# Performance work log

Measured on AMD Instinct MI355X. Metric: run time of the kernel, lower is better.

The kernel has to match this reference:

```python
import jax, jax.numpy as jnp
import numpy as np

B, S, D, H = 4, 2048, 1024, 16
HD = D // H


def setup_inputs() -> dict:
    key = jax.random.key(0)
    k1, k2, k3 = jax.random.split(key, 3)
    x = jax.random.normal(k1, (B, S, D), dtype=jnp.float32)
    w_qkv = jax.random.normal(k2, (D, 3 * D), dtype=jnp.float32) * (1.0 / np.sqrt(D))
    w_out = jax.random.normal(k3, (D, D), dtype=jnp.float32) * (1.0 / np.sqrt(D))
    return {"x": x, "w_qkv": w_qkv, "w_out": w_out}


def reference(x, w_qkv, w_out):
    bsz, seq_len, d = x.shape
    qkv = x @ w_qkv  # [B, S, 3D]
    q, k, v = jnp.split(qkv, 3, axis=-1)
    # [B, H, S, HD]
    q = q.reshape(bsz, seq_len, H, HD).transpose(0, 2, 1, 3)
    k = k.reshape(bsz, seq_len, H, HD).transpose(0, 2, 1, 3)
    v = v.reshape(bsz, seq_len, H, HD).transpose(0, 2, 1, 3)
    scale = 1.0 / np.sqrt(HD)
    scores = jnp.einsum('bhqd,bhkd->bhqk', q, k) * scale  # [B, H, S, S]
    causal = jnp.tril(jnp.ones((seq_len, seq_len), dtype=bool))
    scores = jnp.where(causal[None, None], scores, -jnp.inf)
    weights = jax.nn.softmax(scores, axis=-1)
    ctx = jnp.einsum('bhqk,bhkd->bhqd', weights, v)
    ctx = ctx.transpose(0, 2, 1, 3).reshape(bsz, seq_len, d)
    return ctx @ w_out
```

## Files before the change

### kernel.cpp

```cpp
#include <hip/hip_runtime.h>
#include <stdint.h>

typedef unsigned short u16;
typedef __attribute__((ext_vector_type(4))) float f32x4;
typedef __attribute__((ext_vector_type(8))) __bf16 bf16x8;
typedef __attribute__((ext_vector_type(8))) u16 u16x8;
typedef __attribute__((ext_vector_type(4))) u16 u16x4;

static constexpr int kB = 4, kS = 2048, kD = 1024, kH = 16, kHD = 64;
static constexpr int M1 = kB * kS;
static constexpr int N1 = 3 * kD;
static constexpr int K1 = kD;

#define SCLF 0.18033688011112042f
#define MFMA16(a, b, c) __builtin_amdgcn_mfma_f32_16x16x32_bf16((a), (b), (c), 0, 0, 0)

union U4 { unsigned u[4]; bf16x8 v; };

__device__ __forceinline__ u16 f2bf(float f) {
  union { float f; uint32_t u; } c; c.f = f;
  uint32_t u = c.u + 0x7FFFu + ((c.u >> 16) & 1u);
  return (u16)(u >> 16);
}

__device__ __forceinline__ unsigned pkbf(float a, float b) {
  union { __bf16 h[2]; unsigned u; } c;
  c.h[0] = (__bf16)a; c.h[1] = (__bf16)b;
  return c.u;
}

__device__ __forceinline__ void gload_lds16(const u16* g, u16* l) {
  __builtin_amdgcn_global_load_lds(
      (const __attribute__((address_space(1))) unsigned int*)g,
      (__attribute__((address_space(3))) unsigned int*)l, 16, 0, 0);
}

__global__ __launch_bounds__(256) void k_cast_x(const float* __restrict__ x,
                                                u16* __restrict__ o) {
  int i = (blockIdx.x * 256 + threadIdx.x) * 4;
  f32x4 v = *(const f32x4*)(x + i);
  u16x4 r;
  r[0] = f2bf(v[0]); r[1] = f2bf(v[1]); r[2] = f2bf(v[2]); r[3] = f2bf(v[3]);
  *(u16x4*)(o + i) = r;
}

__global__ __launch_bounds__(256) void k_transpose_cast(const float* __restrict__ w,
                                                        u16* __restrict__ wt,
                                                        int K, int N) {
  __shared__ float t[32][33];
  const int n0 = blockIdx.x * 32, k0 = blockIdx.y * 32;
  const int tx = threadIdx.x & 31, ty = threadIdx.x >> 5;
  for (int r = ty; r < 32; r += 8)
    t[r][tx] = w[(size_t)(k0 + r) * N + n0 + tx];
  __syncthreads();
  for (int r = ty; r < 32; r += 8)
    wt[(size_t)(n0 + r) * K + k0 + tx] = f2bf(t[tx][r]);
}

template <int MODE>
__global__ __launch_bounds__(256) void k_gemm_bt(const u16* __restrict__ A,
                                                 const u16* __restrict__ BT,
                                                 u16* __restrict__ obf,
                                                 float* __restrict__ of,
                                                 int M, int N, int K) {
  typedef __attribute__((ext_vector_type(4))) float f4;
  __shared__ __align__(16) u16 As[128 * 32];
  __shared__ __align__(16) u16 Bs[128 * 32];
  const int tid = threadIdx.x;
  const int wave = tid >> 6, lane = tid & 63;
  const int l15 = lane & 15, l16 = lane >> 4;

  const int bid = blockIdx.y * gridDim.x + blockIdx.x;
  const int qch = (gridDim.x * gridDim.y) >> 3;
  const int swz = (bid & 7) * qch + (bid >> 3);
  const int row0 = (swz / gridDim.x) * 128, col0 = (swz % gridDim.x) * 128;
  const int wm = (wave >> 1) * 64, wn = (wave & 1) * 64;

  f4 acc[4][4];
#pragma unroll
  for (int i = 0; i < 4; ++i)
#pragma unroll
    for (int j = 0; j < 4; ++j) acc[i][j] = f4{0.f, 0.f, 0.f, 0.f};

  const int e0 = wave * 512 + lane * 8;
  const int r0 = e0 >> 5, c0 = e0 & 31;
  const int e1 = e0 + 2048;
  const int r1 = e1 >> 5, c1 = e1 & 31;
  const u16* Ab = A + (size_t)row0 * K;
  const u16* Bb = BT + (size_t)col0 * K;

  for (int kt = 0; kt < K; kt += 32) {
    gload_lds16(Ab + (size_t)r0 * K + kt + c0, &As[wave * 512]);
    gload_lds16(Ab + (size_t)r1 * K + kt + c1, &As[2048 + wave * 512]);
    gload_lds16(Bb + (size_t)r0 * K + kt + c0, &Bs[wave * 512]);
    gload_lds16(Bb + (size_t)r1 * K + kt + c1, &Bs[2048 + wave * 512]);
    __syncthreads();
    bf16x8 af[4], bfv[4];
#pragma unroll
    for (int f = 0; f < 4; ++f) {
      af[f]  = *(const bf16x8*)&As[(wm + f * 16 + l15) * 32 + l16 * 8];
      bfv[f] = *(const bf16x8*)&Bs[(wn + f * 16 + l15) * 32 + l16 * 8];
    }
#pragma unroll
    for (int fm = 0; fm < 4; ++fm)
#pragma unroll
      for (int fn = 0; fn < 4; ++fn)
        acc[fm][fn] = MFMA16(af[fm], bfv[fn], acc[fm][fn]);
    __syncthreads();
  }

#pragma unroll
  for (int fm = 0; fm < 4; ++fm)
#pragma unroll
    for (int fn = 0; fn < 4; ++fn) {
      const int n = col0 + wn + fn * 16 + l15;
#pragma unroll
      for (int j = 0; j < 4; ++j) {
        const int m = row0 + wm + fm * 16 + l16 * 4 + j;
        float v = acc[fm][fn][j];
        if constexpr (MODE == 0) {
          const int which = n >> 10, d = n & 1023;
          const int h = d >> 6, hd = d & 63;
          const int b = m >> 11, s = m & 2047;
          if (which == 0) v *= SCLF;
          obf[((((size_t)which * 4 + b) * 16 + h) * 2048 + s) * 64 + hd] = f2bf(v);
        } else {
          of[(size_t)m * N + n] = v;
        }
      }
    }
}

__global__ __launch_bounds__(512, 4) void k_attn(const u16* __restrict__ Qg,
                                                 const u16* __restrict__ Kg,
                                                 const u16* __restrict__ Vg,
                                                 u16* __restrict__ ctx) {
  __shared__ __align__(16) u16 Ks[2][64 * 64];
  __shared__ __align__(16) unsigned Vt[2][2048];

  const int bid = blockIdx.x;
  const int xcd = bid & 7, i2 = bid >> 3;
  const int bh = xcd * 8 + (i2 & 7);
  const int p = i2 >> 3;
  const int bb = bh >> 4, hh = bh & 15;
  const int tid = threadIdx.x;
  const int wave = tid >> 6, lane = tid & 63;
  const int l15 = lane & 15, l16 = lane >> 4;

  const u16* Qb = Qg + (size_t)bh * kS * kHD;
  const u16* Kb = Kg + (size_t)bh * kS * kHD;
  const u16* Vb = Vg + (size_t)bh * kS * kHD;

  const int kkey = tid >> 3, ksl = tid & 7;
  const int do4 = tid & 15, kp = tid >> 4;
  const int srcA = ((l16 & 1) << 5) + l15;
  const int srcB = srcA + 16;
  const bool lo16 = (l16 < 2);

  unsigned voff[4];
#pragma unroll
  for (int i = 0; i < 4; ++i) {
    const int d = do4 * 4 + i;
    voff[i] = d * 32 + (kp ^ ((((d & 7) ^ (d >> 3))) << 2));
  }
  const u16* ksrc = Kb + (size_t)kkey * 64 + (ksl ^ (kkey & 7)) * 8;

  for (int phase = 0; phase < 2; ++phase) {
    const int qsup = phase ? (15 - p) : p;
    const int qstart = qsup * 128 + wave * 16;
    const int ntiles = 2 * qsup + 2;

    bf16x8 bq[2];
#pragma unroll
    for (int ds = 0; ds < 2; ++ds)
      bq[ds] = *(const bf16x8*)(Qb + (size_t)(qstart + l15) * 64 + ds * 32 + l16 * 8);

    f32x4 acc[4];
#pragma unroll
    for (int i = 0; i < 4; ++i) acc[i] = f32x4{0.f, 0.f, 0.f, 0.f};
    float mrow = -3e38f, lrowh = 0.f;

    __syncthreads();

    u16x4 va, vb;
    {
      const u16* vs = Vb + (size_t)(2 * kp) * 64 + do4 * 4;
      va = *(const u16x4*)vs; vb = *(const u16x4*)(vs + 64);
    }
#pragma unroll
    for (int i = 0; i < 4; ++i)
      Vt[0][voff[i]] = (unsigned)va[i] | ((unsigned)vb[i] << 16);
    {
      const u16* vs = Vb + (size_t)(64 + 2 * kp) * 64 + do4 * 4;
      va = *(const u16x4*)vs; vb = *(const u16x4*)(vs + 64);
    }
    gload_lds16(ksrc, &Ks[0][wave * 512]);

    for (int t = 0; t < ntiles; ++t) {
      const int kv0 = t * 64;
      __syncthreads();

      if (t + 1 < ntiles) {
        const int nb = (t + 1) & 1;
#pragma unroll
        for (int i = 0; i < 4; ++i)
          Vt[nb][voff[i]] = (unsigned)va[i] | ((unsigned)vb[i] << 16);
        gload_lds16(ksrc + (size_t)(t + 1) * 64 * 64, &Ks[nb][wave * 512]);
        if (t + 2 < ntiles) {
          const u16* vs = Vb + (size_t)((t + 2) * 64 + 2 * kp) * 64 + do4 * 4;
          va = *(const u16x4*)vs; vb = *(const u16x4*)(vs + 64);
        }
      }

      if (kv0 > qstart + 15) continue;

      const u16* Ksb = &Ks[t & 1][0];
      const unsigned* Vtb = &Vt[t & 1][0];
      const int qv = qstart + l15;

#pragma unroll
      for (int c = 0; c < 2; ++c) {
        const int kb = kv0 + 32 * c;
        if (kb > qstart + 15) continue;

        f32x4 st0 = f32x4{0.f, 0.f, 0.f, 0.f}, st1 = st0;
        __builtin_amdgcn_s_setprio(1);
#pragma unroll
        for (int ds = 0; ds < 2; ++ds) {
          const int slot = ((ds * 4 + l16) ^ (l15 & 7)) * 8;
          bf16x8 ak0 = *(const bf16x8*)&Ksb[(c * 32 + l15) * 64 + slot];
          st0 = MFMA16(ak0, bq[ds], st0);
          bf16x8 ak1 = *(const bf16x8*)&Ksb[(c * 32 + 16 + l15) * 64 + slot];
          st1 = MFMA16(ak1, bq[ds], st1);
        }
        __builtin_amdgcn_s_setprio(0);

        float tl;
        if (kb + 31 > qstart) {
#pragma unroll
          for (int j = 0; j < 4; ++j) {
            const int key = kb + l16 * 4 + j;
            st0[j] = (key <= qv) ? st0[j] : -3e38f;
            st1[j] = (key + 16 <= qv) ? st1[j] : -3e38f;
          }
        }
        tl = fmaxf(fmaxf(fmaxf(st0[0], st0[1]), fmaxf(st0[2], st0[3])),
                   fmaxf(fmaxf(st1[0], st1[1]), fmaxf(st1[2], st1[3])));

        float mn;
        if (__all(tl <= mrow + 8.0f)) {
          mn = mrow;
        } else {
          float tj = fmaxf(tl, __shfl_xor(tl, 16, 64));
          tj = fmaxf(tj, __shfl_xor(tj, 32, 64));
          mn = fmaxf(mrow, tj);
          const float al = exp2f(mrow - mn);
          mrow = mn;
          lrowh *= al;
#pragma unroll
          for (int i = 0; i < 4; ++i)
#pragma unroll
            for (int j = 0; j < 4; ++j) acc[i][j] *= al;
        }

#pragma unroll
        for (int j = 0; j < 4; ++j) {
          st0[j] = exp2f(st0[j] - mn);
          st1[j] = exp2f(st1[j] - mn);
        }
        lrowh += ((st0[0] + st0[1]) + (st0[2] + st0[3])) +
                 ((st1[0] + st1[1]) + (st1[2] + st1[3]));

        const unsigned a0  = pkbf(st0[0], st0[1]), a0b = pkbf(st0[2], st0[3]);
        const unsigned a1  = pkbf(st1[0], st1[1]), a1b = pkbf(st1[2], st1[3]);
        const unsigned sA0  = __shfl(a0, srcA, 64),  sA0b = __shfl(a0b, srcA, 64);
        const unsigned sB0  = __shfl(a0, srcB, 64),  sB0b = __shfl(a0b, srcB, 64);
        const unsigned sA1  = __shfl(a1, srcA, 64),  sA1b = __shfl(a1b, srcA, 64);
        const unsigned sB1  = __shfl(a1, srcB, 64),  sB1b = __shfl(a1b, srcB, 64);
        U4 f;
        f.u[0] = lo16 ? sA0 : sA1;  f.u[1] = lo16 ? sA0b : sA1b;
        f.u[2] = lo16 ? sB0 : sB1;  f.u[3] = lo16 ? sB0b : sB1b;

        __builtin_amdgcn_s_setprio(1);
#pragma unroll
        for (int dg = 0; dg < 4; ++dg) {
          const int d = dg * 16 + l15;
          const int addr = d * 32 + ((c * 16 + l16 * 4) ^ ((((d & 7) ^ (d >> 3))) << 2));
          const bf16x8 vf = *(const bf16x8*)&Vtb[addr];
          acc[dg] = MFMA16(vf, f.v, acc[dg]);
        }
        __builtin_amdgcn_s_setprio(0);
      }
    }

    float l2 = lrowh + __shfl_xor(lrowh, 16, 64);
    const float lrow = l2 + __shfl_xor(l2, 32, 64);
    const float rl = 1.0f / lrow;
    u16* orow = ctx + ((size_t)bb * kS + (qstart + l15)) * kD + hh * 64;
#pragma unroll
    for (int dg = 0; dg < 4; ++dg) {
      u16x4 pk;
#pragma unroll
      for (int j = 0; j < 4; ++j) pk[j] = f2bf(acc[dg][j] * rl);
      *(u16x4*)&orow[dg * 16 + l16 * 4] = pk;
    }
  }
}

extern "C" void kernel_launch(void* const* d_in, const int* in_sizes, int n_in,
                              void* d_out, int out_size, void* d_ws, size_t ws_size,
                              hipStream_t stream) {
  const float* x     = (const float*)d_in[0];
  const float* w_qkv = (const float*)d_in[1];
  const float* w_out = (const float*)d_in[2];
  float* out = (float*)d_out;

  u16* ws    = (u16*)d_ws;
  u16* x_bf  = ws;
  u16* wqkvT = x_bf + (size_t)M1 * K1;
  u16* woutT = wqkvT + (size_t)N1 * K1;
  u16* qkv   = woutT + (size_t)kD * kD;
  u16* ctx   = qkv + (size_t)3 * kB * kH * kS * kHD;

  k_cast_x<<<M1 * K1 / 1024, 256, 0, stream>>>(x, x_bf);
  k_transpose_cast<<<dim3(N1 / 32, K1 / 32), 256, 0, stream>>>(w_qkv, wqkvT, K1, N1);
  k_transpose_cast<<<dim3(kD / 32, kD / 32), 256, 0, stream>>>(w_out, woutT, kD, kD);

  k_gemm_bt<0><<<dim3(N1 / 128, M1 / 128), 256, 0, stream>>>(x_bf, wqkvT, qkv, nullptr,
                                                             M1, N1, K1);

  const u16* Qg = qkv;
  const u16* Kg = qkv + (size_t)kB * kH * kS * kHD;
  const u16* Vg = qkv + (size_t)2 * kB * kH * kS * kHD;
  k_attn<<<dim3(512), 512, 0, stream>>>(Qg, Kg, Vg, ctx);

  k_gemm_bt<1><<<dim3(kD / 128, M1 / 128), 256, 0, stream>>>(ctx, woutT, nullptr, out,
                                                             M1, kD, K1);
}
```

Baseline: 206.1 us.

## Rewrite GEMM with 128x256 tiles, triple-buffered async LDS loads and swizzle

Restructures the projection GEMMs to use 512-thread blocks with 128x256 output tiles, a K-step of 64, and a three-stage LDS ring. Loads go straight to LDS and are overlapped with MFMA compute using explicit vmcnt waits and a single barrier per step. An XOR swizzle on LDS columns avoids bank conflicts, and MFMA priority is raised. The aim is to hide global memory latency and raise arithmetic intensity per block, at the cost of higher LDS use (144KB per block) and fewer blocks in flight.

```diff
diff --git a/kernel.cpp b/kernel.cpp
--- a/kernel.cpp
+++ b/kernel.cpp
@@ -58,55 +58,91 @@
 }
 
 template <int MODE>
-__global__ __launch_bounds__(256) void k_gemm_bt(const u16* __restrict__ A,
+__global__ __launch_bounds__(512) void k_gemm_bt(const u16* __restrict__ A,
                                                  const u16* __restrict__ BT,
                                                  u16* __restrict__ obf,
                                                  float* __restrict__ of,
                                                  int M, int N, int K) {
-  typedef __attribute__((ext_vector_type(4))) float f4;
-  __shared__ __align__(16) u16 As[128 * 32];
-  __shared__ __align__(16) u16 Bs[128 * 32];
+  __shared__ __align__(16) u16 Asb[3][128 * 64];
+  __shared__ __align__(16) u16 Bsb[3][256 * 64];
+
   const int tid = threadIdx.x;
   const int wave = tid >> 6, lane = tid & 63;
   const int l15 = lane & 15, l16 = lane >> 4;
 
-  const int bid = blockIdx.y * gridDim.x + blockIdx.x;
-  const int qch = (gridDim.x * gridDim.y) >> 3;
+  const int bid = blockIdx.x;
+  const int qch = gridDim.x >> 3;
   const int swz = (bid & 7) * qch + (bid >> 3);
-  const int row0 = (swz / gridDim.x) * 128, col0 = (swz % gridDim.x) * 128;
-  const int wm = (wave >> 1) * 64, wn = (wave & 1) * 64;
-
-  f4 acc[4][4];
+  const int ntN = N >> 8;
+  const int row0 = (swz / ntN) * 128, col0 = (swz % ntN) * 256;
+  const int wm = (wave >> 2) * 64, wn = (wave & 3) * 64;
+
+  f32x4 acc[4][4];
 #pragma unroll
   for (int i = 0; i < 4; ++i)
 #pragma unroll
-    for (int j = 0; j < 4; ++j) acc[i][j] = f4{0.f, 0.f, 0.f, 0.f};
-
-  const int e0 = wave * 512 + lane * 8;
-  const int r0 = e0 >> 5, c0 = e0 & 31;
-  const int e1 = e0 + 2048;
-  const int r1 = e1 >> 5, c1 = e1 & 31;
-  const u16* Ab = A + (size_t)row0 * K;
-  const u16* Bb = BT + (size_t)col0 * K;
-
-  for (int kt = 0; kt < K; kt += 32) {
-    gload_lds16(Ab + (size_t)r0 * K + kt + c0, &As[wave * 512]);
-    gload_lds16(Ab + (size_t)r1 * K + kt + c1, &As[2048 + wave * 512]);
-    gload_lds16(Bb + (size_t)r0 * K + kt + c0, &Bs[wave * 512]);
-    gload_lds16(Bb + (size_t)r1 * K + kt + c1, &Bs[2048 + wave * 512]);
-    __syncthreads();
-    bf16x8 af[4], bfv[4];
-#pragma unroll
-    for (int f = 0; f < 4; ++f) {
-      af[f]  = *(const bf16x8*)&As[(wm + f * 16 + l15) * 32 + l16 * 8];
-      bfv[f] = *(const bf16x8*)&Bs[(wn + f * 16 + l15) * 32 + l16 * 8];
-    }
-#pragma unroll
-    for (int fm = 0; fm < 4; ++fm)
-#pragma unroll
-      for (int fn = 0; fn < 4; ++fn)
-        acc[fm][fn] = MFMA16(af[fm], bfv[fn], acc[fm][fn]);
-    __syncthreads();
+    for (int j = 0; j < 4; ++j) acc[i][j] = f32x4{0.f, 0.f, 0.f, 0.f};
+
+  const int lr = lane >> 3, ls = lane & 7;
+  const u16* srcA[2];
+  u16 rowAswz[2];
+#pragma unroll
+  for (int j = 0; j < 2; ++j) {
+    const int r = (wave * 2 + j) * 8 + lr;
+    srcA[j] = A + (size_t)(row0 + r) * K + (ls ^ (r & 7)) * 8;
+  }
+  const u16* srcB[4];
+#pragma unroll
+  for (int j = 0; j < 4; ++j) {
+    const int r = (wave * 4 + j) * 8 + lr;
+    srcB[j] = BT + (size_t)(col0 + r) * K + (ls ^ (r & 7)) * 8;
+  }
+
+  const int nT = K >> 6;
+
+#define STAGE(t)                                                        \
+  {                                                                     \
+    const int buf_ = (t) % 3;                                           \
+    const int kt_ = (t) * 64;                                           \
+    _Pragma("unroll")                                                   \
+    for (int j = 0; j < 2; ++j)                                         \
+      gload_lds16(srcA[j] + kt_, &Asb[buf_][(wave * 2 + j) * 512]);     \
+    _Pragma("unroll")                                                   \
+    for (int j = 0; j < 4; ++j)                                         \
+      gload_lds16(srcB[j] + kt_, &Bsb[buf_][(wave * 4 + j) * 512]);     \
+  }
+
+  STAGE(0);
+  STAGE(1);
+
+  for (int t = 0; t < nT; ++t) {
+    if (t + 1 < nT) asm volatile("s_waitcnt vmcnt(6)" ::: "memory");
+    else            asm volatile("s_waitcnt vmcnt(0)" ::: "memory");
+    __builtin_amdgcn_s_barrier();
+    __builtin_amdgcn_sched_barrier(0);
+
+    if (t + 2 < nT) STAGE(t + 2);
+
+    const u16* As = &Asb[t % 3][0];
+    const u16* Bs = &Bsb[t % 3][0];
+#pragma unroll
+    for (int kk = 0; kk < 2; ++kk) {
+      bf16x8 af[4], bfv[4];
+#pragma unroll
+      for (int f = 0; f < 4; ++f) {
+        const int ra = wm + f * 16 + l15;
+        af[f] = *(const bf16x8*)&As[ra * 64 + (((kk * 4 + l16) ^ (ra & 7)) * 8)];
+        const int rb = wn + f * 16 + l15;
+        bfv[f] = *(const bf16x8*)&Bs[rb * 64 + (((kk * 4 + l16) ^ (rb & 7)) * 8)];
+      }
+      __builtin_amdgcn_s_setprio(1);
+#pragma unroll
+      for (int fm = 0; fm < 4; ++fm)
+#pragma unroll
+        for (int fn = 0; fn < 4; ++fn)
+          acc[fm][fn] = MFMA16(af[fm], bfv[fn], acc[fm][fn]);
+      __builtin_amdgcn_s_setprio(0);
+    }
   }
 
 #pragma unroll
@@ -129,6 +165,7 @@
         }
       }
     }
+#undef STAGE
 }
 
 __global__ __launch_bounds__(512, 4) void k_attn(const u16* __restrict__ Qg,
@@ -326,14 +363,14 @@
   k_transpose_cast<<<dim3(N1 / 32, K1 / 32), 256, 0, stream>>>(w_qkv, wqkvT, K1, N1);
   k_transpose_cast<<<dim3(kD / 32, kD / 32), 256, 0, stream>>>(w_out, woutT, kD, kD);
 
-  k_gemm_bt<0><<<dim3(N1 / 128, M1 / 128), 256, 0, stream>>>(x_bf, wqkvT, qkv, nullptr,
-                                                             M1, N1, K1);
+  k_gemm_bt<0><<<dim3(768), 512, 0, stream>>>(x_bf, wqkvT, qkv, nullptr,
+                                              M1, N1, K1);
 
   const u16* Qg = qkv;
   const u16* Kg = qkv + (size_t)kB * kH * kS * kHD;
   const u16* Vg = qkv + (size_t)2 * kB * kH * kS * kHD;
   k_attn<<<dim3(512), 512, 0, stream>>>(Qg, Kg, Vg, ctx);
 
-  k_gemm_bt<1><<<dim3(kD / 128, M1 / 128), 256, 0, stream>>>(ctx, woutT, nullptr, out,
-                                                             M1, kD, K1);
-}
+  k_gemm_bt<1><<<dim3(256), 512, 0, stream>>>(ctx, woutT, nullptr, out,
+                                              M1, kD, K1);
+}
```

Result: no change. 207.3 us (+0.6%).
